# Optimization experiments

Measured on AMD Instinct MI355X. Metric: run time of the kernel, lower is better.

The kernel has to match this reference:

```python
import jax, jax.numpy as jnp
import numpy as np

N = 100000
E = 1600000
IN_C = 128
HID = 128
OUT_C = 2
EPS = 1e-5


def gcn_conv(x, src, dst, norm, W, b, num_nodes):
    # PyG GCNConv: linear transform then symmetric-normalized scatter-add
    h = x @ W                                  # [N, out]
    msg = h[src] * norm[:, None]               # [E+N, out] gather
    out = jax.ops.segment_sum(msg, dst, num_segments=num_nodes)
    return out + b


def batchnorm_eval(x, gamma, beta, rm, rv):
    inv = gamma / jnp.sqrt(rv + EPS)
    return (x - rm) * inv + beta


def setup_inputs() -> dict:
    key = jax.random.key(0)
    ks = jax.random.split(key, 16)
    x = jax.random.normal(ks[0], (N, IN_C), dtype=jnp.float32)
    edge_index = jax.random.randint(ks[1], (2, E), 0, N, dtype=jnp.int32)
    s = 1.0 / np.sqrt(IN_C)
    W1 = jax.random.uniform(ks[2], (IN_C, HID), jnp.float32, -s, s)
    b1 = jnp.zeros((HID,), jnp.float32)
    g1 = jnp.ones((HID,), jnp.float32)
    be1 = jnp.zeros((HID,), jnp.float32)
    rm1 = jax.random.normal(ks[3], (HID,), jnp.float32) * 0.1
    rv1 = jax.random.uniform(ks[4], (HID,), jnp.float32, 0.5, 1.5)
    s2 = 1.0 / np.sqrt(HID)
    W2 = jax.random.uniform(ks[5], (HID, HID), jnp.float32, -s2, s2)
    b2 = jnp.zeros((HID,), jnp.float32)
    g2 = jnp.ones((HID,), jnp.float32)
    be2 = jnp.zeros((HID,), jnp.float32)
    rm2 = jax.random.normal(ks[6], (HID,), jnp.float32) * 0.1
    rv2 = jax.random.uniform(ks[7], (HID,), jnp.float32, 0.5, 1.5)
    W3 = jax.random.uniform(ks[8], (HID, OUT_C), jnp.float32, -s2, s2)
    b3 = jnp.zeros((OUT_C,), jnp.float32)
    return {"x": x, "edge_index": edge_index,
            "W1": W1, "b1": b1, "g1": g1, "be1": be1, "rm1": rm1, "rv1": rv1,
            "W2": W2, "b2": b2, "g2": g2, "be2": be2, "rm2": rm2, "rv2": rv2,
            "W3": W3, "b3": b3}


def reference(x, edge_index, W1, b1, g1, be1, rm1, rv1,
              W2, b2, g2, be2, rm2, rv2, W3, b3):
    num_nodes = x.shape[0]
    loops = jnp.arange(num_nodes, dtype=edge_index.dtype)
    src = jnp.concatenate([edge_index[0], loops])   # add self loops
    dst = jnp.concatenate([edge_index[1], loops])
    deg = jax.ops.segment_sum(jnp.ones_like(dst, dtype=x.dtype), dst,
                              num_segments=num_nodes)
    dinv = jax.lax.rsqrt(deg)                        # deg >= 1 with self loops
    norm = dinv[src] * dinv[dst]                     # [E+N]

    h = gcn_conv(x, src, dst, norm, W1, b1, num_nodes)
    h = jax.nn.relu(batchnorm_eval(h, g1, be1, rm1, rv1))
    h = gcn_conv(h, src, dst, norm, W2, b2, num_nodes)
    h = jax.nn.relu(batchnorm_eval(h, g2, be2, rm2, rv2))
    out = gcn_conv(h, src, dst, norm, W3, b3, num_nodes)
    return out
```

## Files before the change

kernel.cpp:

```cpp
#include <hip/hip_runtime.h>

#define NN 100000
#define EE 1600000
#define CH 128

typedef _Float16 h2 __attribute__((ext_vector_type(2)));
typedef _Float16 h8 __attribute__((ext_vector_type(8)));
typedef float f32x4 __attribute__((ext_vector_type(4)));

#define S_NODES 512
#define NBUCK 196
#define CAP_E 10240


__global__ __launch_bounds__(256) void k_passA(const int* __restrict__ src, const int* __restrict__ dst,
                                               int* __restrict__ gcur, int* __restrict__ eb) {
    __shared__ int hist[NBUCK];
    __shared__ int curL[NBUCK];
    for (int t = threadIdx.x; t < NBUCK; t += 256) hist[t] = 0;
    __syncthreads();
    int base = blockIdx.x * 4096;
    int pk[16], bk[16];
#pragma unroll
    for (int j = 0; j < 16; ++j) {
        int i = base + threadIdx.x + 256 * j;
        if (i < EE) {
            int s = src[i], d = dst[i];
            bk[j] = d >> 9;
            pk[j] = (s << 9) | (d & 511);
            atomicAdd(&hist[bk[j]], 1);
        } else bk[j] = -1;
    }
    __syncthreads();
    for (int t = threadIdx.x; t < NBUCK; t += 256) {
        int h = hist[t];
        curL[t] = (h > 0) ? atomicAdd(&gcur[t], h) : 0;
    }
    __syncthreads();
#pragma unroll
    for (int j = 0; j < 16; ++j) {
        if (bk[j] >= 0) {
            int pos = atomicAdd(&curL[bk[j]], 1);
            if (pos < CAP_E) eb[bk[j] * CAP_E + pos] = pk[j];
        }
    }
}


__global__ __launch_bounds__(256) void k_bscan_prep(const int* __restrict__ gcur, int* __restrict__ bbase,
                                                    int* __restrict__ rp,
                                                    const float* __restrict__ W1, const float* __restrict__ W2,
                                                    _Float16* __restrict__ Wt1, _Float16* __restrict__ Wt2,
                                                    const float* __restrict__ b1, const float* __restrict__ g1,
                                                    const float* __restrict__ be1, const float* __restrict__ rm1,
                                                    const float* __restrict__ rv1,
                                                    const float* __restrict__ b2, const float* __restrict__ g2,
                                                    const float* __restrict__ be2, const float* __restrict__ rm2,
                                                    const float* __restrict__ rv2,
                                                    float* __restrict__ sc1, float* __restrict__ sh1,
                                                    float* __restrict__ sc2, float* __restrict__ sh2) {
    int bid = blockIdx.x, tid = threadIdx.x;
    if (bid == 0) {
        __shared__ int ts[256];
        int nn = (tid < NBUCK) ? min(S_NODES, NN - tid * S_NODES) : 0;
        int v = (tid < NBUCK) ? (min(gcur[tid], CAP_E) + nn) : 0;
        ts[tid] = v; __syncthreads();
        for (int off = 1; off < 256; off <<= 1) {
            int u = (tid >= off) ? ts[tid - off] : 0;
            __syncthreads();
            ts[tid] += u;
            __syncthreads();
        }
        if (tid < NBUCK) bbase[tid] = ts[tid] - v;
        if (tid == 0) rp[NN] = EE + NN;
    } else if (bid <= 64) {
        int r = (bid - 1) * 2 + (tid >> 7);
        int k = tid & 127;
        Wt1[r * 128 + k] = (_Float16)W1[k * 128 + r];
    } else if (bid <= 128) {
        int r = (bid - 65) * 2 + (tid >> 7);
        int k = tid & 127;
        Wt2[r * 128 + k] = (_Float16)W2[k * 128 + r];
    } else {
        if (tid < 128) {
            float sv = g1[tid] * rsqrtf(rv1[tid] + 1e-5f);
            sc1[tid] = sv;
            sh1[tid] = (b1[tid] - rm1[tid]) * sv + be1[tid];
        } else {
            int t = tid - 128;
            float sv = g2[t] * rsqrtf(rv2[t] + 1e-5f);
            sc2[t] = sv;
            sh2[t] = (b2[t] - rm2[t]) * sv + be2[t];
        }
    }
}


__global__ __launch_bounds__(256) void k_passB(const int* __restrict__ gcur, const int* __restrict__ eb,
                                               const int* __restrict__ bbase, int* __restrict__ rp,
                                               float* __restrict__ dinv, int* __restrict__ col) {
    __shared__ int c[S_NODES];
    __shared__ int excl[S_NODES];
    __shared__ int cur[S_NODES];
    __shared__ int ts[256];
    __shared__ int stage[CAP_E + S_NODES];
    int bId = blockIdx.x;
    int nbase = bId * S_NODES;
    int tid = threadIdx.x;
    c[tid] = 0; c[tid + 256] = 0;
    __syncthreads();
    int n = min(gcur[bId], CAP_E);
    const int* e = eb + (size_t)bId * CAP_E;
    for (int i = tid; i < n; i += 256) atomicAdd(&c[e[i] & 511], 1);
    __syncthreads();
    int n0 = nbase + 2 * tid, n1 = n0 + 1;
    int v0 = (n0 < NN) ? c[2 * tid] + 1 : 0;
    int v1 = (n1 < NN) ? c[2 * tid + 1] + 1 : 0;
    int s = v0 + v1;
    ts[tid] = s; __syncthreads();
    for (int off = 1; off < 256; off <<= 1) {
        int u = (tid >= off) ? ts[tid - off] : 0;
        __syncthreads();
        ts[tid] += u;
        __syncthreads();
    }
    int ex = ts[tid] - s;
    int base = bbase[bId];
    excl[2 * tid] = ex; excl[2 * tid + 1] = ex + v0;
    cur[2 * tid] = ex;  cur[2 * tid + 1] = ex + v0;
    if (n0 < NN) { rp[n0] = base + ex;      dinv[n0] = rsqrtf((float)v0); }
    if (n1 < NN) { rp[n1] = base + ex + v0; dinv[n1] = rsqrtf((float)v1); }
    __syncthreads();
    for (int i = tid; i < n; i += 256) {
        int pe = e[i];
        int pos = atomicAdd(&cur[pe & 511], 1);
        stage[pos] = pe >> 9;
    }
    {
        int t0 = 2 * tid, t1 = 2 * tid + 1;
        if (n0 < NN) stage[excl[t0] + c[t0]] = n0;
        if (n1 < NN) stage[excl[t1] + c[t1]] = n1;
    }
    __syncthreads();
    int total = ts[255];
    for (int i = tid; i < total; i += 256) col[base + i] = stage[i];
}


template <bool F32IN>
__global__ __launch_bounds__(256) void k_gemm_mfma(const void* __restrict__ Ain,
                                                   const _Float16* __restrict__ Wt,
                                                   const float* __restrict__ dinv,
                                                   _Float16* __restrict__ C) {
    __shared__ _Float16 Wl[CH * CH];
    {
        const float4* wg = (const float4*)Wt;
#pragma unroll
        for (int i = 0; i < 8; ++i) {
            int chunk = i * 256 + threadIdx.x;
            int row = chunk >> 4, slot = chunk & 15;
            float4 v = wg[chunk];
            *(float4*)((char*)Wl + row * 256 + ((slot ^ (row & 15)) * 16)) = v;
        }
    }
    __syncthreads();
    int lane = threadIdx.x & 63;
    int l15 = lane & 15, lhi = lane >> 4;
    int row0 = blockIdx.x * 64 + (threadIdx.x >> 6) * 16;
    if (row0 >= NN) return;

    h8 afrag[4];
    if (F32IN) {
        const float* Arow = (const float*)Ain + (size_t)(row0 + l15) * CH + lhi * 8;
#pragma unroll
        for (int ks = 0; ks < 4; ++ks) {
            float4 a = *(const float4*)(Arow + ks * 32);
            float4 b = *(const float4*)(Arow + ks * 32 + 4);
            h8 o;
            o[0] = (_Float16)a.x; o[1] = (_Float16)a.y; o[2] = (_Float16)a.z; o[3] = (_Float16)a.w;
            o[4] = (_Float16)b.x; o[5] = (_Float16)b.y; o[6] = (_Float16)b.z; o[7] = (_Float16)b.w;
            afrag[ks] = o;
        }
    } else {
        const _Float16* Arow = (const _Float16*)Ain + (size_t)(row0 + l15) * CH + lhi * 8;
#pragma unroll
        for (int ks = 0; ks < 4; ++ks) afrag[ks] = *(const h8*)(Arow + ks * 32);
    }

    f32x4 acc[8] = {};
#pragma unroll
    for (int ks = 0; ks < 4; ++ks) {
        int slot = ks * 4 + lhi;
#pragma unroll
        for (int c = 0; c < 8; ++c) {
            int brow = c * 16 + l15;
            h8 b = *(const h8*)((char*)Wl + brow * 256 + ((slot ^ (brow & 15)) * 16));
            acc[c] = __builtin_amdgcn_mfma_f32_16x16x32_f16(afrag[ks], b, acc[c], 0, 0, 0);
        }
    }
    float dv[4];
#pragma unroll
    for (int j = 0; j < 4; ++j) dv[j] = dinv[row0 + lhi * 4 + j];
#pragma unroll
    for (int c = 0; c < 8; ++c)
#pragma unroll
        for (int j = 0; j < 4; ++j) {
            float v = acc[c][j] * dv[j];
            C[(size_t)(row0 + lhi * 4 + j) * CH + c * 16 + l15] = (_Float16)v;
        }
}


__global__ __launch_bounds__(256) void k_agg128h(const _Float16* __restrict__ h, const int* __restrict__ rp,
                                                 const int* __restrict__ col, const float* __restrict__ dinv,
                                                 const float* __restrict__ sc, const float* __restrict__ sh,
                                                 _Float16* __restrict__ out) {
    int node = blockIdx.x * 4 + (threadIdx.x >> 6);
    if (node >= NN) return;
    node = __builtin_amdgcn_readfirstlane(node);
    int lane = threadIdx.x & 63;
    int beg = rp[node], end = rp[node + 1];
    float ax = 0.f, ay = 0.f;
    int e = beg;
    for (; e + 8 <= end; e += 8) {
        int s0 = col[e], s1 = col[e + 1], s2 = col[e + 2], s3 = col[e + 3];
        int s4 = col[e + 4], s5 = col[e + 5], s6 = col[e + 6], s7 = col[e + 7];
        h2 v0 = *(const h2*)(h + (size_t)s0 * CH + lane * 2);
        h2 v1 = *(const h2*)(h + (size_t)s1 * CH + lane * 2);
        h2 v2 = *(const h2*)(h + (size_t)s2 * CH + lane * 2);
        h2 v3 = *(const h2*)(h + (size_t)s3 * CH + lane * 2);
        h2 v4 = *(const h2*)(h + (size_t)s4 * CH + lane * 2);
        h2 v5 = *(const h2*)(h + (size_t)s5 * CH + lane * 2);
        h2 v6 = *(const h2*)(h + (size_t)s6 * CH + lane * 2);
        h2 v7 = *(const h2*)(h + (size_t)s7 * CH + lane * 2);
        ax += ((float)v0[0] + (float)v1[0]) + ((float)v2[0] + (float)v3[0])
            + ((float)v4[0] + (float)v5[0]) + ((float)v6[0] + (float)v7[0]);
        ay += ((float)v0[1] + (float)v1[1]) + ((float)v2[1] + (float)v3[1])
            + ((float)v4[1] + (float)v5[1]) + ((float)v6[1] + (float)v7[1]);
    }
    if (e + 4 <= end) {
        int s0 = col[e], s1 = col[e + 1], s2 = col[e + 2], s3 = col[e + 3];
        h2 v0 = *(const h2*)(h + (size_t)s0 * CH + lane * 2);
        h2 v1 = *(const h2*)(h + (size_t)s1 * CH + lane * 2);
        h2 v2 = *(const h2*)(h + (size_t)s2 * CH + lane * 2);
        h2 v3 = *(const h2*)(h + (size_t)s3 * CH + lane * 2);
        ax += ((float)v0[0] + (float)v1[0]) + ((float)v2[0] + (float)v3[0]);
        ay += ((float)v0[1] + (float)v1[1]) + ((float)v2[1] + (float)v3[1]);
        e += 4;
    }
    for (; e < end; ++e) {
        int s0 = col[e];
        h2 v0 = *(const h2*)(h + (size_t)s0 * CH + lane * 2);
        ax += (float)v0[0];
        ay += (float)v0[1];
    }
    float dvn = dinv[node];
    int c = lane * 2;
    float2 scv = *(const float2*)(sc + c);
    float2 shv = *(const float2*)(sh + c);
    float o0 = fmaxf(fmaf(ax * dvn, scv.x, shv.x), 0.f);
    float o1 = fmaxf(fmaf(ay * dvn, scv.y, shv.y), 0.f);
    h2 o; o[0] = (_Float16)o0; o[1] = (_Float16)o1;
    *(h2*)(out + (size_t)node * CH + c) = o;
}


__global__ __launch_bounds__(256) void k_gemm_out(const _Float16* __restrict__ A, const float* __restrict__ W3,
                                                  const float* __restrict__ dinv, float* __restrict__ H3) {
    __shared__ float w3s[256];
    w3s[threadIdx.x] = W3[threadIdx.x];
    __syncthreads();
    int n = blockIdx.x * 256 + threadIdx.x;
    if (n >= NN) return;
    const h8* ar = (const h8*)(A + (size_t)n * CH);
    float a0 = 0.f, a1 = 0.f;
#pragma unroll
    for (int kb = 0; kb < 16; ++kb) {
        h8 a = ar[kb];
#pragma unroll
        for (int j = 0; j < 8; ++j) {
            float av = (float)a[j];
            int k = kb * 8 + j;
            a0 += av * w3s[k * 2];
            a1 += av * w3s[k * 2 + 1];
        }
    }
    float dv = dinv[n];
    *(float2*)(H3 + (size_t)n * 2) = make_float2(a0 * dv, a1 * dv);
}

__global__ __launch_bounds__(256) void k_agg_out(const float* __restrict__ H3, const int* __restrict__ rp,
                                                 const int* __restrict__ col, const float* __restrict__ dinv,
                                                 const float* __restrict__ b3, float* __restrict__ out) {
    int n = blockIdx.x * 256 + threadIdx.x;
    if (n >= NN) return;
    int beg = rp[n], end = rp[n + 1];
    float a0 = 0.f, a1 = 0.f;
    for (int e = beg; e < end; ++e) {
        int s = col[e];
        float2 hv = *(const float2*)(H3 + (size_t)s * 2);
        a0 += hv.x;
        a1 += hv.y;
    }
    float dv = dinv[n];
    out[(size_t)n * 2 + 0] = fmaf(a0, dv, b3[0]);
    out[(size_t)n * 2 + 1] = fmaf(a1, dv, b3[1]);
}


extern "C" void kernel_launch(void* const* d_in, const int* in_sizes, int n_in,
                              void* d_out, int out_size, void* d_ws, size_t ws_size,
                              hipStream_t stream) {
    const float* x  = (const float*)d_in[0];
    const int* ei   = (const int*)d_in[1];
    const int* src  = ei;
    const int* dst  = ei + EE;
    const float* W1 = (const float*)d_in[2];
    const float* b1 = (const float*)d_in[3];
    const float* g1 = (const float*)d_in[4];
    const float* be1 = (const float*)d_in[5];
    const float* rm1 = (const float*)d_in[6];
    const float* rv1 = (const float*)d_in[7];
    const float* W2 = (const float*)d_in[8];
    const float* b2 = (const float*)d_in[9];
    const float* g2 = (const float*)d_in[10];
    const float* be2 = (const float*)d_in[11];
    const float* rm2 = (const float*)d_in[12];
    const float* rv2 = (const float*)d_in[13];
    const float* W3 = (const float*)d_in[14];
    const float* b3 = (const float*)d_in[15];
    float* out = (float*)d_out;

    char* p = (char*)d_ws;
    auto carve = [&](size_t bytes) -> void* {
        void* r = (void*)p;
        p += (bytes + 255) & ~(size_t)255;
        return r;
    };
    int* rp     = (int*)carve((size_t)(NN + 1) * 4);
    float* dinv = (float*)carve((size_t)NN * 4);
    int* col    = (int*)carve((size_t)(EE + NN) * 4);
    int* bbase  = (int*)carve(256 * 4);
    float* sc1  = (float*)carve(128 * 4);
    float* sh1  = (float*)carve(128 * 4);
    float* sc2  = (float*)carve(128 * 4);
    float* sh2  = (float*)carve(128 * 4);
    _Float16* bufA = (_Float16*)carve((size_t)NN * CH * 2);
    _Float16* bufB = (_Float16*)carve((size_t)NN * CH * 2);
    _Float16* Wt1  = (_Float16*)carve(128 * 128 * 2);
    _Float16* Wt2  = (_Float16*)carve(128 * 128 * 2);
    float* h3   = (float*)carve((size_t)NN * 2 * 4);

    int* eb   = (int*)bufA;
    int* gcur = eb + (size_t)NBUCK * CAP_E;

    hipMemsetAsync(gcur, 0, (size_t)NBUCK * 4, stream);

    k_passA<<<(EE + 4095) / 4096, 256, 0, stream>>>(src, dst, gcur, eb);
    k_bscan_prep<<<130, 256, 0, stream>>>(gcur, bbase, rp,
                                          W1, W2, Wt1, Wt2,
                                          b1, g1, be1, rm1, rv1,
                                          b2, g2, be2, rm2, rv2,
                                          sc1, sh1, sc2, sh2);
    k_passB<<<NBUCK, 256, 0, stream>>>(gcur, eb, bbase, rp, dinv, col);

    k_gemm_mfma<true><<<(NN + 63) / 64, 256, 0, stream>>>(x, Wt1, dinv, bufA);
    k_agg128h<<<(NN + 3) / 4, 256, 0, stream>>>(bufA, rp, col, dinv, sc1, sh1, bufB);
    k_gemm_mfma<false><<<(NN + 63) / 64, 256, 0, stream>>>(bufB, Wt2, dinv, bufA);
    k_agg128h<<<(NN + 3) / 4, 256, 0, stream>>>(bufA, rp, col, dinv, sc2, sh2, bufB);
    k_gemm_out<<<(NN + 255) / 256, 256, 0, stream>>>(bufB, W3, dinv, h3);
    k_agg_out<<<(NN + 255) / 256, 256, 0, stream>>>(h3, rp, col, dinv, b3, out);
}
```

Before: 226.3 us.

## Split hidden features into two 64-channel slices and aggregate per slice

Hidden activations are now stored as two column slices of 64 fp16 channels, each laid out contiguously per node, and the GEMM, aggregation and output GEMM kernels index that layout. The aggregation kernel launches twice as many blocks, one per slice; each wave splits its 64 lanes into two halves that gather alternate edges from 128-byte rows and are combined with a cross-lane shuffle. The aim is a smaller gather working set per pass, better L2 locality and more memory-level parallelism. In exchange, col and rp are read twice, and the GEMM stores are more strided.

```diff
diff --git a/kernel.cpp b/kernel.cpp
--- a/kernel.cpp
+++ b/kernel.cpp
@@ -11,6 +11,8 @@
 #define S_NODES 512
 #define NBUCK 196
 #define CAP_E 10240
+
+#define SLICE_STRIDE ((size_t)NN * 64)
 
 
 __global__ __launch_bounds__(256) void k_passA(const int* __restrict__ src, const int* __restrict__ dst,
@@ -182,9 +184,13 @@
             afrag[ks] = o;
         }
     } else {
-        const _Float16* Arow = (const _Float16*)Ain + (size_t)(row0 + l15) * CH + lhi * 8;
-#pragma unroll
-        for (int ks = 0; ks < 4; ++ks) afrag[ks] = *(const h8*)(Arow + ks * 32);
+        const _Float16* Ah = (const _Float16*)Ain;
+#pragma unroll
+        for (int ks = 0; ks < 4; ++ks) {
+            int ch = ks * 32 + lhi * 8;
+            afrag[ks] = *(const h8*)(Ah + (size_t)(ch >> 6) * SLICE_STRIDE
+                                     + (size_t)(row0 + l15) * 64 + (ch & 63));
+        }
     }
 
     f32x4 acc[8] = {};
@@ -202,66 +208,76 @@
 #pragma unroll
     for (int j = 0; j < 4; ++j) dv[j] = dinv[row0 + lhi * 4 + j];
 #pragma unroll
-    for (int c = 0; c < 8; ++c)
+    for (int c = 0; c < 8; ++c) {
+        int colIdx = c * 16 + l15;
+        _Float16* Cd = C + (size_t)(colIdx >> 6) * SLICE_STRIDE + (colIdx & 63);
 #pragma unroll
         for (int j = 0; j < 4; ++j) {
             float v = acc[c][j] * dv[j];
-            C[(size_t)(row0 + lhi * 4 + j) * CH + c * 16 + l15] = (_Float16)v;
-        }
-}
-
-
-__global__ __launch_bounds__(256) void k_agg128h(const _Float16* __restrict__ h, const int* __restrict__ rp,
-                                                 const int* __restrict__ col, const float* __restrict__ dinv,
-                                                 const float* __restrict__ sc, const float* __restrict__ sh,
-                                                 _Float16* __restrict__ out) {
-    int node = blockIdx.x * 4 + (threadIdx.x >> 6);
+            Cd[(size_t)(row0 + lhi * 4 + j) * 64] = (_Float16)v;
+        }
+    }
+}
+
+
+__global__ __launch_bounds__(256) void k_aggs6(const _Float16* __restrict__ h, const int* __restrict__ rp,
+                                               const int* __restrict__ col, const float* __restrict__ dinv,
+                                               const float* __restrict__ sc, const float* __restrict__ sh,
+                                               _Float16* __restrict__ out) {
+    int slice = blockIdx.x & 1;
+    int node = (blockIdx.x >> 1) * 4 + (threadIdx.x >> 6);
     if (node >= NN) return;
     node = __builtin_amdgcn_readfirstlane(node);
     int lane = threadIdx.x & 63;
+    int esub = lane >> 5;
+    int cp = lane & 31;
     int beg = rp[node], end = rp[node + 1];
-    float ax = 0.f, ay = 0.f;
+    const _Float16* hs = h + (size_t)slice * SLICE_STRIDE;
+    float ax = 0.f, ay = 0.f, bx = 0.f, by = 0.f;
     int e = beg;
     for (; e + 8 <= end; e += 8) {
-        int s0 = col[e], s1 = col[e + 1], s2 = col[e + 2], s3 = col[e + 3];
+        int s0 = col[e],     s1 = col[e + 1], s2 = col[e + 2], s3 = col[e + 3];
         int s4 = col[e + 4], s5 = col[e + 5], s6 = col[e + 6], s7 = col[e + 7];
-        h2 v0 = *(const h2*)(h + (size_t)s0 * CH + lane * 2);
-        h2 v1 = *(const h2*)(h + (size_t)s1 * CH + lane * 2);
-        h2 v2 = *(const h2*)(h + (size_t)s2 * CH + lane * 2);
-        h2 v3 = *(const h2*)(h + (size_t)s3 * CH + lane * 2);
-        h2 v4 = *(const h2*)(h + (size_t)s4 * CH + lane * 2);
-        h2 v5 = *(const h2*)(h + (size_t)s5 * CH + lane * 2);
-        h2 v6 = *(const h2*)(h + (size_t)s6 * CH + lane * 2);
-        h2 v7 = *(const h2*)(h + (size_t)s7 * CH + lane * 2);
-        ax += ((float)v0[0] + (float)v1[0]) + ((float)v2[0] + (float)v3[0])
-            + ((float)v4[0] + (float)v5[0]) + ((float)v6[0] + (float)v7[0]);
-        ay += ((float)v0[1] + (float)v1[1]) + ((float)v2[1] + (float)v3[1])
-            + ((float)v4[1] + (float)v5[1]) + ((float)v6[1] + (float)v7[1]);
-    }
-    if (e + 4 <= end) {
-        int s0 = col[e], s1 = col[e + 1], s2 = col[e + 2], s3 = col[e + 3];
-        h2 v0 = *(const h2*)(h + (size_t)s0 * CH + lane * 2);
-        h2 v1 = *(const h2*)(h + (size_t)s1 * CH + lane * 2);
-        h2 v2 = *(const h2*)(h + (size_t)s2 * CH + lane * 2);
-        h2 v3 = *(const h2*)(h + (size_t)s3 * CH + lane * 2);
-        ax += ((float)v0[0] + (float)v1[0]) + ((float)v2[0] + (float)v3[0]);
-        ay += ((float)v0[1] + (float)v1[1]) + ((float)v2[1] + (float)v3[1]);
-        e += 4;
-    }
-    for (; e < end; ++e) {
-        int s0 = col[e];
-        h2 v0 = *(const h2*)(h + (size_t)s0 * CH + lane * 2);
+        int i0 = esub ? s1 : s0;
+        int i1 = esub ? s3 : s2;
+        int i2 = esub ? s5 : s4;
+        int i3 = esub ? s7 : s6;
+        h2 v0 = *(const h2*)(hs + (size_t)i0 * 64 + cp * 2);
+        h2 v1 = *(const h2*)(hs + (size_t)i1 * 64 + cp * 2);
+        h2 v2 = *(const h2*)(hs + (size_t)i2 * 64 + cp * 2);
+        h2 v3 = *(const h2*)(hs + (size_t)i3 * 64 + cp * 2);
+        ax += (float)v0[0] + (float)v1[0];
+        ay += (float)v0[1] + (float)v1[1];
+        bx += (float)v2[0] + (float)v3[0];
+        by += (float)v2[1] + (float)v3[1];
+    }
+    for (; e + 2 <= end; e += 2) {
+        int s0 = col[e], s1 = col[e + 1];
+        int i0 = esub ? s1 : s0;
+        h2 v0 = *(const h2*)(hs + (size_t)i0 * 64 + cp * 2);
         ax += (float)v0[0];
         ay += (float)v0[1];
     }
-    float dvn = dinv[node];
-    int c = lane * 2;
-    float2 scv = *(const float2*)(sc + c);
-    float2 shv = *(const float2*)(sh + c);
-    float o0 = fmaxf(fmaf(ax * dvn, scv.x, shv.x), 0.f);
-    float o1 = fmaxf(fmaf(ay * dvn, scv.y, shv.y), 0.f);
-    h2 o; o[0] = (_Float16)o0; o[1] = (_Float16)o1;
-    *(h2*)(out + (size_t)node * CH + c) = o;
+    if (e < end) {
+        int s0 = col[e];
+        h2 v0 = *(const h2*)(hs + (size_t)s0 * 64 + cp * 2);
+        float m = (esub == 0) ? 1.f : 0.f;
+        ax = fmaf((float)v0[0], m, ax);
+        ay = fmaf((float)v0[1], m, ay);
+    }
+    ax += bx; ay += by;
+    ax += __shfl_xor(ax, 32);
+    ay += __shfl_xor(ay, 32);
+    if (esub == 0) {
+        float dvn = dinv[node];
+        int c = slice * 64 + cp * 2;
+        float2 scv = *(const float2*)(sc + c);
+        float2 shv = *(const float2*)(sh + c);
+        float o0 = fmaxf(fmaf(ax * dvn, scv.x, shv.x), 0.f);
+        float o1 = fmaxf(fmaf(ay * dvn, scv.y, shv.y), 0.f);
+        h2 o; o[0] = (_Float16)o0; o[1] = (_Float16)o1;
+        *(h2*)(out + (size_t)slice * SLICE_STRIDE + (size_t)node * 64 + cp * 2) = o;
+    }
 }
 
 
@@ -272,15 +288,15 @@
     __syncthreads();
     int n = blockIdx.x * 256 + threadIdx.x;
     if (n >= NN) return;
-    const h8* ar = (const h8*)(A + (size_t)n * CH);
     float a0 = 0.f, a1 = 0.f;
 #pragma unroll
     for (int kb = 0; kb < 16; ++kb) {
-        h8 a = ar[kb];
+        int ch = kb * 8;
+        h8 a = *(const h8*)(A + (size_t)(ch >> 6) * SLICE_STRIDE + (size_t)n * 64 + (ch & 63));
 #pragma unroll
         for (int j = 0; j < 8; ++j) {
             float av = (float)a[j];
-            int k = kb * 8 + j;
+            int k = ch + j;
             a0 += av * w3s[k * 2];
             a1 += av * w3s[k * 2 + 1];
         }
@@ -364,10 +380,11 @@
                                           sc1, sh1, sc2, sh2);
     k_passB<<<NBUCK, 256, 0, stream>>>(gcur, eb, bbase, rp, dinv, col);
 
+    int aggBlocks = 2 * ((NN + 3) / 4);
     k_gemm_mfma<true><<<(NN + 63) / 64, 256, 0, stream>>>(x, Wt1, dinv, bufA);
-    k_agg128h<<<(NN + 3) / 4, 256, 0, stream>>>(bufA, rp, col, dinv, sc1, sh1, bufB);
+    k_aggs6<<<aggBlocks, 256, 0, stream>>>(bufA, rp, col, dinv, sc1, sh1, bufB);
     k_gemm_mfma<false><<<(NN + 63) / 64, 256, 0, stream>>>(bufB, Wt2, dinv, bufA);
-    k_agg128h<<<(NN + 3) / 4, 256, 0, stream>>>(bufA, rp, col, dinv, sc2, sh2, bufB);
+    k_aggs6<<<aggBlocks, 256, 0, stream>>>(bufA, rp, col, dinv, sc2, sh2, bufB);
     k_gemm_out<<<(NN + 255) / 256, 256, 0, stream>>>(bufB, W3, dinv, h3);
     k_agg_out<<<(NN + 255) / 256, 256, 0, stream>>>(h3, rp, col, dinv, b3, out);
 }
```

Result: slower. 266.7 us (+17.8%).

## Fuse layer-2 aggregation with W3 projection; vectorize edge loads in bucketing pass

Applied to the files above, without the earlier changes.

The second 128-channel aggregation kernel now applies batchnorm+ReLU and immediately projects onto W3 with a wavefront shuffle reduction, writing only the 2-wide pre-scaled output. This removes the fp16 128-channel intermediate write and its re-read by a separate GEMM kernel, plus one launch. Separately, the edge bucketing pass loads src/dst as int4 contiguous chunks per thread instead of strided scalars. The shuffle reduction adds per-node cross-lane work, and the contiguous-per-thread layout changes coalescing and relies on EE being a multiple of 16.

```diff
diff --git a/kernel.cpp b/kernel.cpp
--- a/kernel.cpp
+++ b/kernel.cpp
@@ -19,17 +19,25 @@
     __shared__ int curL[NBUCK];
     for (int t = threadIdx.x; t < NBUCK; t += 256) hist[t] = 0;
     __syncthreads();
-    int base = blockIdx.x * 4096;
+    int base = blockIdx.x * 4096 + threadIdx.x * 16;
     int pk[16], bk[16];
-#pragma unroll
-    for (int j = 0; j < 16; ++j) {
-        int i = base + threadIdx.x + 256 * j;
-        if (i < EE) {
-            int s = src[i], d = dst[i];
-            bk[j] = d >> 9;
-            pk[j] = (s << 9) | (d & 511);
-            atomicAdd(&hist[bk[j]], 1);
-        } else bk[j] = -1;
+    if (base < EE) {
+        const int4* sv = (const int4*)(src + base);
+        const int4* dv = (const int4*)(dst + base);
+#pragma unroll
+        for (int q = 0; q < 4; ++q) {
+            int4 s4 = sv[q], d4 = dv[q];
+            int j = q * 4;
+            bk[j + 0] = d4.x >> 9; pk[j + 0] = (s4.x << 9) | (d4.x & 511);
+            bk[j + 1] = d4.y >> 9; pk[j + 1] = (s4.y << 9) | (d4.y & 511);
+            bk[j + 2] = d4.z >> 9; pk[j + 2] = (s4.z << 9) | (d4.z & 511);
+            bk[j + 3] = d4.w >> 9; pk[j + 3] = (s4.w << 9) | (d4.w & 511);
+        }
+#pragma unroll
+        for (int j = 0; j < 16; ++j) atomicAdd(&hist[bk[j]], 1);
+    } else {
+#pragma unroll
+        for (int j = 0; j < 16; ++j) bk[j] = -1;
     }
     __syncthreads();
     for (int t = threadIdx.x; t < NBUCK; t += 256) {
@@ -265,29 +273,67 @@
 }
 
 
-__global__ __launch_bounds__(256) void k_gemm_out(const _Float16* __restrict__ A, const float* __restrict__ W3,
-                                                  const float* __restrict__ dinv, float* __restrict__ H3) {
-    __shared__ float w3s[256];
-    w3s[threadIdx.x] = W3[threadIdx.x];
-    __syncthreads();
-    int n = blockIdx.x * 256 + threadIdx.x;
-    if (n >= NN) return;
-    const h8* ar = (const h8*)(A + (size_t)n * CH);
-    float a0 = 0.f, a1 = 0.f;
-#pragma unroll
-    for (int kb = 0; kb < 16; ++kb) {
-        h8 a = ar[kb];
-#pragma unroll
-        for (int j = 0; j < 8; ++j) {
-            float av = (float)a[j];
-            int k = kb * 8 + j;
-            a0 += av * w3s[k * 2];
-            a1 += av * w3s[k * 2 + 1];
-        }
-    }
-    float dv = dinv[n];
-    *(float2*)(H3 + (size_t)n * 2) = make_float2(a0 * dv, a1 * dv);
-}
+__global__ __launch_bounds__(256) void k_agg_w3(const _Float16* __restrict__ h, const int* __restrict__ rp,
+                                                const int* __restrict__ col, const float* __restrict__ dinv,
+                                                const float* __restrict__ sc, const float* __restrict__ sh,
+                                                const float* __restrict__ W3, float* __restrict__ H3) {
+    int node = blockIdx.x * 4 + (threadIdx.x >> 6);
+    if (node >= NN) return;
+    node = __builtin_amdgcn_readfirstlane(node);
+    int lane = threadIdx.x & 63;
+    int beg = rp[node], end = rp[node + 1];
+    float ax = 0.f, ay = 0.f;
+    int e = beg;
+    for (; e + 8 <= end; e += 8) {
+        int s0 = col[e], s1 = col[e + 1], s2 = col[e + 2], s3 = col[e + 3];
+        int s4 = col[e + 4], s5 = col[e + 5], s6 = col[e + 6], s7 = col[e + 7];
+        h2 v0 = *(const h2*)(h + (size_t)s0 * CH + lane * 2);
+        h2 v1 = *(const h2*)(h + (size_t)s1 * CH + lane * 2);
+        h2 v2 = *(const h2*)(h + (size_t)s2 * CH + lane * 2);
+        h2 v3 = *(const h2*)(h + (size_t)s3 * CH + lane * 2);
+        h2 v4 = *(const h2*)(h + (size_t)s4 * CH + lane * 2);
+        h2 v5 = *(const h2*)(h + (size_t)s5 * CH + lane * 2);
+        h2 v6 = *(const h2*)(h + (size_t)s6 * CH + lane * 2);
+        h2 v7 = *(const h2*)(h + (size_t)s7 * CH + lane * 2);
+        ax += ((float)v0[0] + (float)v1[0]) + ((float)v2[0] + (float)v3[0])
+            + ((float)v4[0] + (float)v5[0]) + ((float)v6[0] + (float)v7[0]);
+        ay += ((float)v0[1] + (float)v1[1]) + ((float)v2[1] + (float)v3[1])
+            + ((float)v4[1] + (float)v5[1]) + ((float)v6[1] + (float)v7[1]);
+    }
+    if (e + 4 <= end) {
+        int s0 = col[e], s1 = col[e + 1], s2 = col[e + 2], s3 = col[e + 3];
+        h2 v0 = *(const h2*)(h + (size_t)s0 * CH + lane * 2);
+        h2 v1 = *(const h2*)(h + (size_t)s1 * CH + lane * 2);
+        h2 v2 = *(const h2*)(h + (size_t)s2 * CH + lane * 2);
+        h2 v3 = *(const h2*)(h + (size_t)s3 * CH + lane * 2);
+        ax += ((float)v0[0] + (float)v1[0]) + ((float)v2[0] + (float)v3[0]);
+        ay += ((float)v0[1] + (float)v1[1]) + ((float)v2[1] + (float)v3[1]);
+        e += 4;
+    }
+    for (; e < end; ++e) {
+        int s0 = col[e];
+        h2 v0 = *(const h2*)(h + (size_t)s0 * CH + lane * 2);
+        ax += (float)v0[0];
+        ay += (float)v0[1];
+    }
+    float dvn = dinv[node];
+    int c = lane * 2;
+    float2 scv = *(const float2*)(sc + c);
+    float2 shv = *(const float2*)(sh + c);
+    float o0 = fmaxf(fmaf(ax * dvn, scv.x, shv.x), 0.f);
+    float o1 = fmaxf(fmaf(ay * dvn, scv.y, shv.y), 0.f);
+    float4 w = *(const float4*)(W3 + c * 2);
+    float a0 = fmaf(o1, w.z, o0 * w.x);
+    float a1 = fmaf(o1, w.w, o0 * w.y);
+#pragma unroll
+    for (int off = 1; off < 64; off <<= 1) {
+        a0 += __shfl_xor(a0, off);
+        a1 += __shfl_xor(a1, off);
+    }
+    if (lane == 0)
+        *(float2*)(H3 + (size_t)node * 2) = make_float2(a0 * dvn, a1 * dvn);
+}
+
 
 __global__ __launch_bounds__(256) void k_agg_out(const float* __restrict__ H3, const int* __restrict__ rp,
                                                  const int* __restrict__ col, const float* __restrict__ dinv,
@@ -367,7 +413,6 @@
     k_gemm_mfma<true><<<(NN + 63) / 64, 256, 0, stream>>>(x, Wt1, dinv, bufA);
     k_agg128h<<<(NN + 3) / 4, 256, 0, stream>>>(bufA, rp, col, dinv, sc1, sh1, bufB);
     k_gemm_mfma<false><<<(NN + 63) / 64, 256, 0, stream>>>(bufB, Wt2, dinv, bufA);
-    k_agg128h<<<(NN + 3) / 4, 256, 0, stream>>>(bufA, rp, col, dinv, sc2, sh2, bufB);
-    k_gemm_out<<<(NN + 255) / 256, 256, 0, stream>>>(bufB, W3, dinv, h3);
+    k_agg_w3<<<(NN + 3) / 4, 256, 0, stream>>>(bufA, rp, col, dinv, sc2, sh2, W3, h3);
     k_agg_out<<<(NN + 255) / 256, 256, 0, stream>>>(h3, rp, col, dinv, b3, out);
 }
```

Result: faster. 216.1 us (-4.5%).
